# Performance work log

Hardware: AMD Instinct MI355X
Metric: run time of the kernel (lower is better)

Reference implementation:

```python
import jax, jax.numpy as jnp
import numpy as np

IN_FEATURES = 4096
PADDED = 4096               # padded_dim == in_features -> no crop
K_HALF = PADDED // 2 + 1    # 2049
K = 1024                    # truncation: only first K half-spectrum coeffs active
BATCH = 8192


def setup_inputs() -> dict:
    key = jax.random.key(0)
    k1, k2, k3, k4 = jax.random.split(key, 4)
    x = jax.random.normal(k1, (BATCH, IN_FEATURES), dtype=jnp.float32)
    w_real = jax.random.normal(k2, (K_HALF,), dtype=jnp.float32) * 0.1
    w_imag = jax.random.normal(k3, (K_HALF,), dtype=jnp.float32) * 0.1
    # DC and Nyquist bins must be real (Hermitian spectrum of a real filter)
    w_imag = w_imag.at[0].set(0.0).at[-1].set(0.0)
    bias = jax.random.normal(k4, (), dtype=jnp.float32) * 0.1
    return {"x": x, "w_real": w_real, "w_imag": w_imag, "bias": bias}


def _fft_full(w_real, w_imag):
    # K-truncated half spectrum -> full Hermitian-symmetric spectrum (PADDED even)
    mask = (jnp.arange(K_HALF) < K).astype(w_real.dtype)
    half = w_real * mask + 1j * (w_imag * mask)            # (K_HALF,) complex
    nyq = half[-1].real[None].astype(half.dtype)           # real Nyquist bin
    full = jnp.concatenate([half[:-1], nyq, jnp.conj(half[1:-1])[::-1]])
    return full                                            # (PADDED,) complex


def reference(x, w_real, w_imag, bias):
    # in_features == padded_dim: no padding, no crop
    fft_full = _fft_full(w_real, w_imag)
    Xf = jnp.fft.fft(x, axis=-1, norm="ortho")             # (B, PADDED) complex
    y = jnp.fft.ifft(Xf * fft_full, axis=-1, norm="ortho").real
    return y + bias                                        # scalar bias (vector_bias=False)
```

## Files before the change

kernel.cpp:

```cpp
#include <hip/hip_runtime.h>

#define NT 256
#define PHYS_PAD(l) ((l) + ((l) >> 5))

template<bool INV>
__device__ __forceinline__ void dft16(float* vr, float* vi) {
    constexpr float C1 = 0.9238795325112867f;
    constexpr float S1 = 0.3826834323650898f;
    constexpr float HF = 0.7071067811865476f;
    const float WR[10] = {1.f,  C1,  HF,  S1, 0.f, 0.f, -HF, 0.f, 0.f, -C1};
    const float WI[10] = {0.f, -S1, -HF, -C1, -1.f, 0.f, -HF, 0.f, 0.f,  S1};

    float ar[16], ai[16];
    #pragma unroll
    for (int jl = 0; jl < 4; ++jl) {
        float x0r = vr[jl],      x0i = vi[jl];
        float x1r = vr[jl + 4],  x1i = vi[jl + 4];
        float x2r = vr[jl + 8],  x2i = vi[jl + 8];
        float x3r = vr[jl + 12], x3i = vi[jl + 12];
        float t0r = x0r + x2r, t0i = x0i + x2i;
        float t1r = x0r - x2r, t1i = x0i - x2i;
        float t2r = x1r + x3r, t2i = x1i + x3i;
        float t3r = x1r - x3r, t3i = x1i - x3i;
        ar[jl]     = t0r + t2r;  ai[jl]     = t0i + t2i;
        ar[jl + 8] = t0r - t2r;  ai[jl + 8] = t0i - t2i;
        if (!INV) {
            ar[jl + 4]  = t1r + t3i;  ai[jl + 4]  = t1i - t3r;
            ar[jl + 12] = t1r - t3i;  ai[jl + 12] = t1i + t3r;
        } else {
            ar[jl + 4]  = t1r - t3i;  ai[jl + 4]  = t1i + t3r;
            ar[jl + 12] = t1r + t3i;  ai[jl + 12] = t1i - t3r;
        }
    }
    #pragma unroll
    for (int k4 = 1; k4 < 4; ++k4) {
        #pragma unroll
        for (int jl = 1; jl < 4; ++jl) {
            const int e = jl * k4;
            float wr = WR[e];
            float wi = INV ? -WI[e] : WI[e];
            const int id = jl + 4 * k4;
            float xr = ar[id], xi = ai[id];
            ar[id] = xr * wr - xi * wi;
            ai[id] = xr * wi + xi * wr;
        }
    }
    #pragma unroll
    for (int k4 = 0; k4 < 4; ++k4) {
        float x0r = ar[4*k4 + 0], x0i = ai[4*k4 + 0];
        float x1r = ar[4*k4 + 1], x1i = ai[4*k4 + 1];
        float x2r = ar[4*k4 + 2], x2i = ai[4*k4 + 2];
        float x3r = ar[4*k4 + 3], x3i = ai[4*k4 + 3];
        float t0r = x0r + x2r, t0i = x0i + x2i;
        float t1r = x0r - x2r, t1i = x0i - x2i;
        float t2r = x1r + x3r, t2i = x1i + x3i;
        float t3r = x1r - x3r, t3i = x1i - x3i;
        vr[k4]     = t0r + t2r;  vi[k4]     = t0i + t2i;
        vr[k4 + 8] = t0r - t2r;  vi[k4 + 8] = t0i - t2i;
        if (!INV) {
            vr[k4 + 4]  = t1r + t3i;  vi[k4 + 4]  = t1i - t3r;
            vr[k4 + 12] = t1r - t3i;  vi[k4 + 12] = t1i + t3r;
        } else {
            vr[k4 + 4]  = t1r - t3i;  vi[k4 + 4]  = t1i + t3r;
            vr[k4 + 12] = t1r + t3i;  vi[k4 + 12] = t1i - t3r;
        }
    }
}

__device__ __forceinline__ void apply_tw_powers(float* vr, float* vi, float wr, float wi) {
    float pr = wr, pi = wi;
    #pragma unroll
    for (int e = 1; e < 16; ++e) {
        float xr = vr[e], xi = vi[e];
        vr[e] = xr * pr - xi * pi;
        vi[e] = xr * pi + xi * pr;
        float nr = pr * wr - pi * wi;
        float ni = pr * wi + pi * wr;
        pr = nr; pi = ni;
    }
}

__global__ __launch_bounds__(NT, 4) void spectral_circulant_r16(
    const float* __restrict__ x,
    const float* __restrict__ w_real,
    const float* __restrict__ w_imag,
    const float* __restrict__ bias_p,
    float* __restrict__ out)
{
    __shared__ float lre[4224];
    __shared__ float lim[4224];

    const int t   = threadIdx.x;
    const int blk = blockIdx.x;

    float vr[16], vi[16];

    const float* __restrict__ xa = x + (size_t)(2 * blk) * 4096;
    const float* __restrict__ xb = xa + 4096;
    #pragma unroll
    for (int j = 0; j < 16; ++j) {
        vr[j] = xa[(j << 8) + t];
        vi[j] = xb[(j << 8) + t];
    }

    dft16<false>(vr, vi);
    float sA, cA;
    __sincosf((float)t * -1.5339807878856412e-3f, &sA, &cA);
    apply_tw_powers(vr, vi, cA, sA);

    {
        const int b0 = t + (t >> 5);
        #pragma unroll
        for (int a = 0; a < 16; ++a) {
            lre[b0 + 264 * a] = vr[a];
            lim[b0 + 264 * a] = vi[a];
        }
    }
    __syncthreads();

    const int ax = t >> 4;
    const int m2 = t & 15;
    const int base1 = 264 * ax + m2;

    #pragma unroll
    for (int q = 0; q < 16; ++q) {
        const int ad = base1 + 16 * q + (q >> 1);
        vr[q] = lre[ad];
        vi[q] = lim[ad];
    }

    dft16<false>(vr, vi);
    float sB, cB;
    __sincosf((float)m2 * -2.454369260617026e-2f, &sB, &cB);
    apply_tw_powers(vr, vi, cB, sB);

    #pragma unroll
    for (int b = 0; b < 16; ++b) {
        const int ad = base1 + 16 * b + (b >> 1);
        lre[ad] = vr[b];
        lim[ad] = vi[b];
    }
    __syncthreads();

    const int a2 = t >> 4;
    const int bb = t & 15;
    const int base2 = 264 * a2 + 16 * bb + (bb >> 1);

    #pragma unroll
    for (int m = 0; m < 16; ++m) {
        vr[m] = lre[base2 + m];
        vi[m] = lim[base2 + m];
    }

    dft16<false>(vr, vi);

    {
        const int c = (bb << 4) | a2;
        const float sc = 1.0f / 4096.0f;
        #pragma unroll
        for (int r3 = 0; r3 < 4; ++r3) {
            const int k = (r3 << 8) + c;
            float hr = w_real[k] * sc;
            float hi = w_imag[k] * sc;
            float xr = vr[r3], xi = vi[r3];
            vr[r3] = xr * hr - xi * hi;
            vi[r3] = xr * hi + xi * hr;
        }
        #pragma unroll
        for (int r3 = 4; r3 < 12; ++r3) {
            vr[r3] = 0.0f; vi[r3] = 0.0f;
        }
        {
            const int idx = 1024 - c;
            const float m = (c > 0) ? sc : 0.0f;
            float hr = w_real[idx] * m;
            float hi = -w_imag[idx] * m;
            float xr = vr[12], xi = vi[12];
            vr[12] = xr * hr - xi * hi;
            vi[12] = xr * hi + xi * hr;
        }
        #pragma unroll
        for (int r3 = 13; r3 < 16; ++r3) {
            const int idx = ((16 - r3) << 8) - c;
            float hr = w_real[idx] * sc;
            float hi = -w_imag[idx] * sc;
            float xr = vr[r3], xi = vi[r3];
            vr[r3] = xr * hr - xi * hi;
            vi[r3] = xr * hi + xi * hr;
        }
    }


    dft16<true>(vr, vi);

    #pragma unroll
    for (int m = 0; m < 16; ++m) {
        lre[base2 + m] = vr[m];
        lim[base2 + m] = vi[m];
    }
    __syncthreads();

    #pragma unroll
    for (int b = 0; b < 16; ++b) {
        const int ad = base1 + 16 * b + (b >> 1);
        vr[b] = lre[ad];
        vi[b] = lim[ad];
    }

    apply_tw_powers(vr, vi, cB, -sB);
    dft16<true>(vr, vi);

    #pragma unroll
    for (int q = 0; q < 16; ++q) {
        const int ad = base1 + 16 * q + (q >> 1);
        lre[ad] = vr[q];
        lim[ad] = vi[q];
    }
    __syncthreads();

    {
        const int b0 = t + (t >> 5);
        #pragma unroll
        for (int a = 0; a < 16; ++a) {
            vr[a] = lre[b0 + 264 * a];
            vi[a] = lim[b0 + 264 * a];
        }
    }

    apply_tw_powers(vr, vi, cA, -sA);
    dft16<true>(vr, vi);

    const float bv = bias_p[0];
    float* __restrict__ oa = out + (size_t)(2 * blk) * 4096;
    float* __restrict__ ob = oa + 4096;
    #pragma unroll
    for (int j = 0; j < 16; ++j) {
        oa[(j << 8) + t] = vr[j] + bv;
        ob[(j << 8) + t] = vi[j] + bv;
    }
}

extern "C" void kernel_launch(void* const* d_in, const int* in_sizes, int n_in,
                              void* d_out, int out_size, void* d_ws, size_t ws_size,
                              hipStream_t stream) {
    (void)in_sizes; (void)n_in; (void)d_ws; (void)ws_size; (void)out_size;
    const float* x      = (const float*)d_in[0];
    const float* w_real = (const float*)d_in[1];
    const float* w_imag = (const float*)d_in[2];
    const float* bias   = (const float*)d_in[3];
    float* out = (float*)d_out;

    spectral_circulant_r16<<<8192 / 2, NT, 0, stream>>>(x, w_real, w_imag, bias, out);
}
```

Baseline: 243.9 us.

## Interleave complex LDS layout, replace middle block barriers with wave barriers

Shared memory now holds real and imaginary parts together as float2 with a new padding scheme, so each complex exchange is a single wider LDS access. The middle transpose is reorganised so each thread's 16 values sit within its own wavefront's region; this lets two __syncthreads be replaced by wave barriers, and the middle-stage reads and writes become float4 accesses. Twiddle power generation is split into odd and even chains to shorten the dependency chain, and output stores use nontemporal hints. The exchange only works if every value a thread reads was written by its own wavefront, and the new padding pattern may introduce bank conflicts.

Result: no change. 240.4 us (-1.4%).

```diff
diff --git a/kernel.cpp b/kernel.cpp
--- a/kernel.cpp
+++ b/kernel.cpp
@@ -1,7 +1,8 @@
 #include <hip/hip_runtime.h>
 
 #define NT 256
-#define PHYS_PAD(l) ((l) + ((l) >> 5))
+
+__device__ __forceinline__ int PH(int l) { return l + 2 * (l >> 4); }
 
 template<bool INV>
 __device__ __forceinline__ void dft16(float* vr, float* vi) {
@@ -68,27 +69,37 @@
 }
 
 __device__ __forceinline__ void apply_tw_powers(float* vr, float* vi, float wr, float wi) {
-    float pr = wr, pi = wi;
-    #pragma unroll
-    for (int e = 1; e < 16; ++e) {
-        float xr = vr[e], xi = vi[e];
-        vr[e] = xr * pr - xi * pi;
-        vi[e] = xr * pi + xi * pr;
-        float nr = pr * wr - pi * wi;
-        float ni = pr * wi + pi * wr;
-        pr = nr; pi = ni;
-    }
-}
-
-__global__ __launch_bounds__(NT, 4) void spectral_circulant_r16(
+    const float w2r = wr * wr - wi * wi;
+    const float w2i = 2.0f * wr * wi;
+    float aor = wr,  aoi = wi;
+    float aer = w2r, aei = w2i;
+    #pragma unroll
+    for (int e = 1; e < 16; e += 2) {
+        { float xr = vr[e], xi = vi[e];
+          vr[e] = xr * aor - xi * aoi;
+          vi[e] = xr * aoi + xi * aor; }
+        if (e + 1 < 16) {
+            float xr = vr[e + 1], xi = vi[e + 1];
+            vr[e + 1] = xr * aer - xi * aei;
+            vi[e + 1] = xr * aei + xi * aer;
+        }
+        if (e + 2 < 16) {
+            float nr = aor * w2r - aoi * w2i, ni = aor * w2i + aoi * w2r;
+            aor = nr; aoi = ni;
+            nr = aer * w2r - aei * w2i; ni = aer * w2i + aei * w2r;
+            aer = nr; aei = ni;
+        }
+    }
+}
+
+__global__ __launch_bounds__(NT, 4) void spectral_circulant_r16v3(
     const float* __restrict__ x,
     const float* __restrict__ w_real,
     const float* __restrict__ w_imag,
     const float* __restrict__ bias_p,
     float* __restrict__ out)
 {
-    __shared__ float lre[4224];
-    __shared__ float lim[4224];
+    __shared__ __align__(16) float2 lds[4606];
 
     const int t   = threadIdx.x;
     const int blk = blockIdx.x;
@@ -109,24 +120,21 @@
     apply_tw_powers(vr, vi, cA, sA);
 
     {
-        const int b0 = t + (t >> 5);
-        #pragma unroll
-        for (int a = 0; a < 16; ++a) {
-            lre[b0 + 264 * a] = vr[a];
-            lim[b0 + 264 * a] = vi[a];
-        }
+        const int tp = t + 2 * (t >> 4);
+        #pragma unroll
+        for (int a = 0; a < 16; ++a)
+            lds[288 * a + tp] = make_float2(vr[a], vi[a]);
     }
     __syncthreads();
 
     const int ax = t >> 4;
     const int m2 = t & 15;
-    const int base1 = 264 * ax + m2;
+    const int base = 288 * ax + m2;
 
     #pragma unroll
     for (int q = 0; q < 16; ++q) {
-        const int ad = base1 + 16 * q + (q >> 1);
-        vr[q] = lre[ad];
-        vi[q] = lim[ad];
+        float2 v = lds[base + 18 * q];
+        vr[q] = v.x; vi[q] = v.y;
     }
 
     dft16<false>(vr, vi);
@@ -135,27 +143,22 @@
     apply_tw_powers(vr, vi, cB, sB);
 
     #pragma unroll
-    for (int b = 0; b < 16; ++b) {
-        const int ad = base1 + 16 * b + (b >> 1);
-        lre[ad] = vr[b];
-        lim[ad] = vi[b];
-    }
-    __syncthreads();
-
-    const int a2 = t >> 4;
-    const int bb = t & 15;
-    const int base2 = 264 * a2 + 16 * bb + (bb >> 1);
-
-    #pragma unroll
-    for (int m = 0; m < 16; ++m) {
-        vr[m] = lre[base2 + m];
-        vi[m] = lim[base2 + m];
+    for (int b = 0; b < 16; ++b)
+        lds[base + 18 * b] = make_float2(vr[b], vi[b]);
+    __builtin_amdgcn_wave_barrier();
+
+    const float4* __restrict__ pfr = (const float4*)&lds[288 * ax + 18 * m2];
+    #pragma unroll
+    for (int m = 0; m < 16; m += 2) {
+        float4 v = pfr[m >> 1];
+        vr[m] = v.x;     vi[m] = v.y;
+        vr[m + 1] = v.z; vi[m + 1] = v.w;
     }
 
     dft16<false>(vr, vi);
 
     {
-        const int c = (bb << 4) | a2;
+        const int c = (m2 << 4) | ax;
         const float sc = 1.0f / 4096.0f;
         #pragma unroll
         for (int r3 = 0; r3 < 4; ++r3) {
@@ -193,37 +196,34 @@
 
     dft16<true>(vr, vi);
 
-    #pragma unroll
-    for (int m = 0; m < 16; ++m) {
-        lre[base2 + m] = vr[m];
-        lim[base2 + m] = vi[m];
-    }
-    __syncthreads();
+    {
+        float4* __restrict__ pfw = (float4*)&lds[288 * ax + 18 * m2];
+        #pragma unroll
+        for (int m = 0; m < 16; m += 2)
+            pfw[m >> 1] = make_float4(vr[m], vi[m], vr[m + 1], vi[m + 1]);
+    }
+    __builtin_amdgcn_wave_barrier();
 
     #pragma unroll
     for (int b = 0; b < 16; ++b) {
-        const int ad = base1 + 16 * b + (b >> 1);
-        vr[b] = lre[ad];
-        vi[b] = lim[ad];
+        float2 v = lds[base + 18 * b];
+        vr[b] = v.x; vi[b] = v.y;
     }
 
     apply_tw_powers(vr, vi, cB, -sB);
     dft16<true>(vr, vi);
 
     #pragma unroll
-    for (int q = 0; q < 16; ++q) {
-        const int ad = base1 + 16 * q + (q >> 1);
-        lre[ad] = vr[q];
-        lim[ad] = vi[q];
-    }
+    for (int q = 0; q < 16; ++q)
+        lds[base + 18 * q] = make_float2(vr[q], vi[q]);
     __syncthreads();
 
     {
-        const int b0 = t + (t >> 5);
+        const int tp = t + 2 * (t >> 4);
         #pragma unroll
         for (int a = 0; a < 16; ++a) {
-            vr[a] = lre[b0 + 264 * a];
-            vi[a] = lim[b0 + 264 * a];
+            float2 v = lds[288 * a + tp];
+            vr[a] = v.x; vi[a] = v.y;
         }
     }
 
@@ -235,8 +235,8 @@
     float* __restrict__ ob = oa + 4096;
     #pragma unroll
     for (int j = 0; j < 16; ++j) {
-        oa[(j << 8) + t] = vr[j] + bv;
-        ob[(j << 8) + t] = vi[j] + bv;
+        __builtin_nontemporal_store(vr[j] + bv, &oa[(j << 8) + t]);
+        __builtin_nontemporal_store(vi[j] + bv, &ob[(j << 8) + t]);
     }
 }
 
@@ -250,5 +250,5 @@
     const float* bias   = (const float*)d_in[3];
     float* out = (float*)d_out;
 
-    spectral_circulant_r16<<<8192 / 2, NT, 0, stream>>>(x, w_real, w_imag, bias, out);
-}
+    spectral_circulant_r16v3<<<8192 / 2, NT, 0, stream>>>(x, w_real, w_imag, bias, out);
+}
```
